# Kernel tuning notes

Hardware: AMD Instinct MI355X
Metric: run time of the kernel (lower is better)

## Reference

```python
import jax, jax.numpy as jnp
import numpy as np

SEQ_LEN = 131072
NUM_NODES = 256
NUM_CAUSES = 16
NUM_FEATURES = 100
NUM_OUTPUTS = 1
NOISE_STD = 0.01


def _build_dag_mask(N, C, p, rng):
    # upper-triangular random adjacency; roots (0..C-1) have no parents;
    # every non-root gets at least one parent (mirrors _build_random_dag)
    A = (rng.random((N, N)) < p) & np.triu(np.ones((N, N), bool), k=1)
    A[:, :C] = False
    for j in range(C, N):
        if not A[:j, j].any():
            A[rng.integers(0, j), j] = True
    return A.astype(np.int32)


def setup_inputs() -> dict:
    key = jax.random.key(0)
    k1, k2, k3 = jax.random.split(key, 3)
    rng = np.random.default_rng(0)
    S, N, C = SEQ_LEN, NUM_NODES, NUM_CAUSES
    causes = jax.random.normal(k1, (S, C), dtype=jnp.float32)
    W = jax.random.normal(k2, (N, N), dtype=jnp.float32)  # edge weights w_ij ~ N(0,1)
    eps = jax.random.normal(k3, (S, N - C), dtype=jnp.float32)  # unit noise, scaled by NOISE_STD
    mask = jnp.asarray(_build_dag_mask(N, C, 0.3, rng))
    act_id = jnp.asarray(rng.integers(0, 4, size=(N - C,)), dtype=jnp.int32)
    # y from a sink-like last node; X from sorted sample of remaining non-root nodes
    y_idx = jnp.asarray([N - 1], dtype=jnp.int64)
    X_idx = jnp.asarray(np.sort(rng.choice(np.arange(C, N - 1), size=NUM_FEATURES, replace=False)), dtype=jnp.int64)
    return {"causes": causes, "W": W, "eps": eps, "mask": mask, "act_id": act_id, "X_idx": X_idx, "y_idx": y_idx}


def reference(causes, W, eps, mask, act_id, X_idx, y_idx):
    S, C = causes.shape
    N = W.shape[0]
    Wm = W * mask.astype(W.dtype)                      # [N,N] masked edge weights (parent i -> node j)
    vals0 = jnp.zeros((S, N), W.dtype).at[:, :C].set(causes)
    Wcols = Wm.T[C:]                                   # [N-C, N] incoming-weight rows per non-root node
    eps_t = eps.T                                      # [N-C, S]
    branches = [lambda z: z, jnp.tanh, jax.nn.relu, jax.nn.sigmoid]

    def step(carry, xs):
        vals, idx = carry
        w_col, e, a = xs
        z = vals @ w_col + jnp.float32(NOISE_STD) * e  # weighted parent sum + noise, [S]
        v = jax.lax.switch(a, branches, z)
        vals = vals.at[:, idx].set(v)
        return (vals, idx + 1), None

    (vals, _), _ = jax.lax.scan(step, (vals0, jnp.int32(C)), (Wcols, eps_t, act_id))
    X = vals[:, X_idx]                                 # [S, num_features]
    y = vals[:, y_idx]                                 # [S, 1]
    bad = jnp.isnan(X).any() | jnp.isnan(y).any()
    X = jnp.where(bad, jnp.float32(0.0), X)
    y = jnp.where(bad, jnp.float32(-100.0), y)
    return X, y[:, 0]                                  # num_outputs == 1 -> squeeze
```

## Files before the change

kernel.cpp:

```cpp
#include <hip/hip_runtime.h>
#include <hip/hip_bf16.h>
#include <hip/hip_fp16.h>


typedef _Float16 half8 __attribute__((ext_vector_type(8)));
typedef float    f32x4 __attribute__((ext_vector_type(4)));

constexpr int S_LEN    = 131072;
constexpr int N_NODES  = 256;
constexpr int N_CAUSES = 16;
constexpr int N_COMP   = 240;
constexpr int N_FEAT   = 100;
constexpr float NOISE  = 0.01f;
constexpr float VSC    = 0.0625f;
constexpr float VSCI   = 16.0f;

constexpr int KE_tab[16]  = {0,32,64,64,96,96,128,128,160,160,192,192,224,224,256,256};
constexpr int OFF_tab[16] = {0,0,1024,3072,5120,8192,11264,15360,19456,24576,29696,
                             35840,41984,49152,56320,64512};

__constant__ int c_KE[16]  = {0,32,64,64,96,96,128,128,160,160,192,192,224,224,256,256};
__constant__ int c_OFF[16] = {0,0,1024,3072,5120,8192,11264,15360,19456,24576,29696,
                              35840,41984,49152,56320,64512};

__device__ _Float16 g_WT[72704];
__device__ float    g_Wtri[15 * 256];

__device__ __forceinline__ bool sniff_binary64(const void* p) {
    const unsigned* u = (const unsigned*)p;
    bool ok = true;
    for (int i = 0; i < 64; ++i) ok = ok && (u[i] <= 1u);
    return ok;
}
__device__ __forceinline__ bool sniff_is_bf16(const void* p) {
    const unsigned* u = (const unsigned*)p;
    bool ok = true;
    for (int i = 0; i < 16; ++i) {
        unsigned e = ((u[i] << 16) >> 23) & 0xffu;
        ok = ok && (e >= 100u) && (e <= 132u);
    }
    return ok;
}
__device__ __forceinline__ float bflo(unsigned u) { return __uint_as_float(u << 16); }
__device__ __forceinline__ float bfhi(unsigned u) { return __uint_as_float(u & 0xffff0000u); }

__device__ __forceinline__ void load16(const void* base, long long off, bool isbf, float* o) {
    if (isbf) {
        const uint4* p = (const uint4*)((const unsigned short*)base + off);
        uint4 a = p[0], b = p[1];
        o[0]=bflo(a.x); o[1]=bfhi(a.x); o[2]=bflo(a.y); o[3]=bfhi(a.y);
        o[4]=bflo(a.z); o[5]=bfhi(a.z); o[6]=bflo(a.w); o[7]=bfhi(a.w);
        o[8]=bflo(b.x); o[9]=bfhi(b.x); o[10]=bflo(b.y); o[11]=bfhi(b.y);
        o[12]=bflo(b.z); o[13]=bfhi(b.z); o[14]=bflo(b.w); o[15]=bfhi(b.w);
    } else {
        const float4* p = (const float4*)((const float*)base + off);
        float4 x0=p[0], x1=p[1], x2=p[2], x3=p[3];
        o[0]=x0.x; o[1]=x0.y; o[2]=x0.z; o[3]=x0.w;
        o[4]=x1.x; o[5]=x1.y; o[6]=x1.z; o[7]=x1.w;
        o[8]=x2.x; o[9]=x2.y; o[10]=x2.z; o[11]=x2.w;
        o[12]=x3.x; o[13]=x3.y; o[14]=x3.z; o[15]=x3.w;
    }
}

__device__ __forceinline__ float hw_exp2(float x) {
    float r; asm("v_exp_f32 %0, %1" : "=v"(r) : "v"(x)); return r;
}
__device__ __forceinline__ float hw_rcp(float x) {
    float r; asm("v_rcp_f32 %0, %1" : "=v"(r) : "v"(x)); return r;
}
__device__ __forceinline__ float fast_tanh(float x) {
    float t = hw_exp2(x * 2.88539008177792681f);
    return 1.0f - 2.0f * hw_rcp(t + 1.0f);
}
__device__ __forceinline__ float fast_sigmoid(float x) {
    return hw_rcp(1.0f + hw_exp2(x * -1.44269504088896341f));
}

__global__ void prep_kernel(const void* __restrict__ A, const void* __restrict__ B) {
    __shared__ int s_mA, s_wbf;
    if (threadIdx.x == 0) {
        s_mA  = sniff_binary64(A) ? 1 : 0;
        s_wbf = sniff_is_bf16(s_mA ? B : A) ? 1 : 0;
    }
    __syncthreads();
    const int*  maskp = (const int*)(s_mA ? A : B);
    const void* Wp    = s_mA ? B : A;
    const int k = blockIdx.x + 1, j0 = 16 * k, KE = c_KE[k], OFF = c_OFF[k];
    const int tid = threadIdx.x;

    for (int n = 0; n < 16; ++n) {
        const int j = j0 + n;
        for (int kk = tid; kk < KE; kk += 256) {
            const int gi = kk * N_NODES + j;
            float w = 0.0f;
            if (maskp[gi])
                w = s_wbf ? __bfloat162float(((const __hip_bfloat16*)Wp)[gi])
                          : ((const float*)Wp)[gi];
            const _Float16 hi = (_Float16)w;
            const _Float16 lo = (_Float16)(w - (float)hi);
            g_WT[OFF + n * KE + kk]           = hi;
            g_WT[OFF + 16 * KE + n * KE + kk] = lo;
        }
    }
    {
        const int l = tid >> 4, i = tid & 15;
        const int gi = (j0 + l) * N_NODES + (j0 + i);
        float w = 0.0f;
        if (l < i && maskp[gi])
            w = s_wbf ? __bfloat162float(((const __hip_bfloat16*)Wp)[gi])
                      : ((const float*)Wp)[gi];
        g_Wtri[(k - 1) * 256 + tid] = w;
    }
}

#define MFMA16(a, b, c) __builtin_amdgcn_mfma_f32_16x16x32_f16((a), (b), (c), 0, 0, 0)

template<int K>
__device__ __forceinline__ void do_chunk(
    const int lane, const long long sg,
    const void* __restrict__ eps, const bool ebf,
    half8 (&vf)[2][8],
    half8 (&bufA)[16], half8 (&bufB)[16],
    float* __restrict__ Zbuf, _Float16* __restrict__ stag,
    const short* __restrict__ xpos, const int* __restrict__ act_id,
    float* __restrict__ wsX,
    float* __restrict__ outX, float* __restrict__ outY, const int yi)
{
    constexpr int j0  = 16 * K;
    constexpr int KE  = KE_tab[K];
    constexpr int NST = KE / 32;

    const int mrow = lane & 15;
    const int quad = lane >> 4;

    half8 (&bc)[16] = *((K & 1) ? &bufA : &bufB);
    half8 (&bn)[16] = *((K & 1) ? &bufB : &bufA);

    float ev[16];
    if (lane < 32)
        load16(eps, sg * (long long)N_COMP + (j0 - N_CAUSES), ebf, ev);

    f32x4 acc0h = {0.f,0.f,0.f,0.f}, acc0l = {0.f,0.f,0.f,0.f};
    f32x4 acc1h = {0.f,0.f,0.f,0.f}, acc1l = {0.f,0.f,0.f,0.f};

    #pragma unroll
    for (int t = 0; t < NST; ++t) {
        acc0h = MFMA16(vf[0][t], bc[t],     acc0h);
        acc1h = MFMA16(vf[1][t], bc[t],     acc1h);
        acc0l = MFMA16(vf[0][t], bc[8 + t], acc0l);
        acc1l = MFMA16(vf[1][t], bc[8 + t], acc1l);
    }

    if constexpr (K < 15) {
        constexpr int KN  = K + 1;
        constexpr int KEn = KE_tab[KN];
        constexpr int NSTn = KEn / 32;
        constexpr int OFFn = OFF_tab[KN];
        const _Float16* __restrict__ bpn = g_WT + OFFn + mrow * KEn + (quad << 3);
        #pragma unroll
        for (int t = 0; t < NSTn; ++t) {
            bn[t]     = *(const half8*)(bpn + (t << 5));
            bn[8 + t] = *(const half8*)(bpn + 16 * KEn + (t << 5));
        }
    }

    {
        const int r0 = quad << 2;
        #pragma unroll
        for (int r = 0; r < 4; ++r) {
            Zbuf[(r0 + r)      * 21 + mrow] = (acc0h[r] + acc0l[r]) * VSCI;
            Zbuf[(16 + r0 + r) * 21 + mrow] = (acc1h[r] + acc1l[r]) * VSCI;
        }
    }
    __builtin_amdgcn_wave_barrier();

    if (lane < 32) {
        float zz[16];
        #pragma unroll
        for (int i = 0; i < 16; ++i)
            zz[i] = Zbuf[lane * 21 + i] + NOISE * ev[i];

        const float* __restrict__ tri = g_Wtri + (K - 1) * 256;
        half8 h0, h1;
        #pragma unroll
        for (int i = 0; i < 16; ++i) {
            float z = zz[i];
            const int a = act_id[j0 - N_CAUSES + i];
            if (a == 1)      z = fast_tanh(z);
            else if (a == 2) z = fmaxf(z, 0.0f);
            else if (a == 3) z = fast_sigmoid(z);
            if (i < 8) h0[i] = (_Float16)(z * VSC);
            else       h1[i - 8] = (_Float16)(z * VSC);
            const int xp = xpos[j0 - N_CAUSES + i];
            if (xp >= 0) {
                if (wsX) wsX[(long long)xp * S_LEN + sg] = z;
                else     outX[xp] = z;
            }
            if (j0 + i == yi) outY[sg] = z;
            #pragma unroll
            for (int j = i + 1; j < 16; ++j)
                zz[j] += tri[(i << 4) + j] * z;
        }
        *(half8*)(stag + lane * 24)     = h0;
        *(half8*)(stag + lane * 24 + 8) = h1;
    }
    __builtin_amdgcn_wave_barrier();

    constexpr int TT = K >> 1;
    constexpr int HB = (K & 1) << 1;
    if (quad == HB || quad == HB + 1) {
        const int boff = (quad - HB) << 3;
        #pragma unroll
        for (int q = 0; q < 2; ++q)
            vf[q][TT] = *(const half8*)(stag + (q * 16 + mrow) * 24 + boff);
    }
    __builtin_amdgcn_wave_barrier();
}

__global__ __launch_bounds__(64, 2)
void scm_kernel(const void* __restrict__ causes,
                const void* __restrict__ eps,
                const int* __restrict__ act_id,
                const void* __restrict__ xidx_raw,
                const int* __restrict__ yidx_raw,
                float* __restrict__ out,
                float* __restrict__ wsX,
                long long ybase) {
    __shared__ __align__(16) float    Zbuf[32 * 21];
    __shared__ __align__(16) _Float16 stag[32 * 24];
    __shared__ short xpos[N_COMP];

    const int lane = threadIdx.x;
    const long long sg = (long long)blockIdx.x * 32 + lane;

    for (int t = lane; t < N_COMP; t += 64) xpos[t] = -1;
    const unsigned long long* x64 = (const unsigned long long*)xidx_raw;
    const int*                x32 = (const int*)xidx_raw;
    const bool is64 = ((x64[0] >> 32) == 0ull);
    __builtin_amdgcn_wave_barrier();
    for (int f = lane; f < N_FEAT; f += 64) {
        const int ix = is64 ? (int)x64[f] : x32[f];
        xpos[ix - N_CAUSES] = (short)f;
    }
    __builtin_amdgcn_wave_barrier();
    const int yi  = yidx_raw[0];
    const bool cbf = sniff_is_bf16(causes);
    const bool ebf = sniff_is_bf16(eps);

    const int mrow = lane & 15;
    const int quad = lane >> 4;

    half8 vz;
    #pragma unroll
    for (int e = 0; e < 8; ++e) vz[e] = (_Float16)0.0f;
    half8 vf[2][8];
    #pragma unroll
    for (int q = 0; q < 2; ++q) {
        #pragma unroll
        for (int t = 0; t < 8; ++t) vf[q][t] = vz;
    }

    half8 bufA[16], bufB[16];
    #pragma unroll
    for (int t = 0; t < 16; ++t) { bufA[t] = vz; bufB[t] = vz; }

    {
        const _Float16* __restrict__ bp1 =
            g_WT + OFF_tab[1] + mrow * KE_tab[1] + (quad << 3);
        bufA[0] = *(const half8*)(bp1);
        bufA[8] = *(const half8*)(bp1 + 16 * KE_tab[1]);
    }

    if (lane < 32) {
        float cv[16];
        load16(causes, sg * (long long)N_CAUSES, cbf, cv);
        half8 c0, c1;
        #pragma unroll
        for (int i = 0; i < 8; ++i) {
            c0[i] = (_Float16)(cv[i] * VSC);
            c1[i] = (_Float16)(cv[8 + i] * VSC);
        }
        *(half8*)(stag + lane * 24)     = c0;
        *(half8*)(stag + lane * 24 + 8) = c1;
    }
    __builtin_amdgcn_wave_barrier();
    if (quad < 2) {
        #pragma unroll
        for (int q = 0; q < 2; ++q)
            vf[q][0] = *(const half8*)(stag + (q * 16 + mrow) * 24 + (quad << 3));
    }
    __builtin_amdgcn_wave_barrier();

    float* outX = out + sg * N_FEAT;
    float* outY = out + ybase;

    do_chunk< 1>(lane, sg, eps, ebf, vf, bufA, bufB, Zbuf, stag, xpos, act_id, wsX, outX, outY, yi);
    do_chunk< 2>(lane, sg, eps, ebf, vf, bufA, bufB, Zbuf, stag, xpos, act_id, wsX, outX, outY, yi);
    do_chunk< 3>(lane, sg, eps, ebf, vf, bufA, bufB, Zbuf, stag, xpos, act_id, wsX, outX, outY, yi);
    do_chunk< 4>(lane, sg, eps, ebf, vf, bufA, bufB, Zbuf, stag, xpos, act_id, wsX, outX, outY, yi);
    do_chunk< 5>(lane, sg, eps, ebf, vf, bufA, bufB, Zbuf, stag, xpos, act_id, wsX, outX, outY, yi);
    do_chunk< 6>(lane, sg, eps, ebf, vf, bufA, bufB, Zbuf, stag, xpos, act_id, wsX, outX, outY, yi);
    do_chunk< 7>(lane, sg, eps, ebf, vf, bufA, bufB, Zbuf, stag, xpos, act_id, wsX, outX, outY, yi);
    do_chunk< 8>(lane, sg, eps, ebf, vf, bufA, bufB, Zbuf, stag, xpos, act_id, wsX, outX, outY, yi);
    do_chunk< 9>(lane, sg, eps, ebf, vf, bufA, bufB, Zbuf, stag, xpos, act_id, wsX, outX, outY, yi);
    do_chunk<10>(lane, sg, eps, ebf, vf, bufA, bufB, Zbuf, stag, xpos, act_id, wsX, outX, outY, yi);
    do_chunk<11>(lane, sg, eps, ebf, vf, bufA, bufB, Zbuf, stag, xpos, act_id, wsX, outX, outY, yi);
    do_chunk<12>(lane, sg, eps, ebf, vf, bufA, bufB, Zbuf, stag, xpos, act_id, wsX, outX, outY, yi);
    do_chunk<13>(lane, sg, eps, ebf, vf, bufA, bufB, Zbuf, stag, xpos, act_id, wsX, outX, outY, yi);
    do_chunk<14>(lane, sg, eps, ebf, vf, bufA, bufB, Zbuf, stag, xpos, act_id, wsX, outX, outY, yi);
    do_chunk<15>(lane, sg, eps, ebf, vf, bufA, bufB, Zbuf, stag, xpos, act_id, wsX, outX, outY, yi);
}

__global__ __launch_bounds__(256)
void xpose_kernel(const float* __restrict__ ws, float* __restrict__ out) {
    __shared__ float tile[64 * 108];
    const int tid = threadIdx.x;
    const long long s0 = (long long)blockIdx.x * 64;
    #pragma unroll
    for (int g = 0; g < 7; ++g) {
        const int idx = g * 256 + tid;
        if (idx < 1600) {
            const int ff = idx >> 4;
            const int sl = idx & 15;
            const float4 v = *(const float4*)(ws + (long long)ff * S_LEN + s0 + sl * 4);
            tile[(sl * 4 + 0) * 108 + ff] = v.x;
            tile[(sl * 4 + 1) * 108 + ff] = v.y;
            tile[(sl * 4 + 2) * 108 + ff] = v.z;
            tile[(sl * 4 + 3) * 108 + ff] = v.w;
        }
    }
    __syncthreads();
    #pragma unroll
    for (int g = 0; g < 7; ++g) {
        const int idx = g * 256 + tid;
        if (idx < 1600) {
            const int s = idx / 25;
            const int j = idx % 25;
            const float4 v = *(const float4*)(tile + s * 108 + j * 4);
            *(float4*)(out + (s0 + s) * N_FEAT + j * 4) = v;
        }
    }
}

extern "C" void kernel_launch(void* const* d_in, const int* in_sizes, int n_in,
                              void* d_out, int out_size, void* d_ws, size_t ws_size,
                              hipStream_t stream) {
    int ic = 0, iw = 1, ie = 2, im = 3, ia = 4, ix = 5, iy = 6;
    int c = -1, e = -1, a = -1, x = -1, y = -1, m1 = -1, m2 = -1;
    for (int i = 0; i < n_in; ++i) {
        switch (in_sizes[i]) {
            case S_LEN * N_CAUSES:   c = i; break;
            case S_LEN * N_COMP:     e = i; break;
            case N_COMP:             a = i; break;
            case N_FEAT:             x = i; break;
            case 1:                  y = i; break;
            case N_NODES * N_NODES:  (m1 < 0 ? m1 : m2) = i; break;
        }
    }
    if (c >= 0 && e >= 0 && a >= 0 && x >= 0 && y >= 0 && m1 >= 0 && m2 >= 0) {
        ic = c; ie = e; ia = a; ix = x; iy = y; iw = m1; im = m2;
    }

    const void* causes = d_in[ic];
    const void* TA     = d_in[iw];
    const void* TB     = d_in[im];
    const void* eps    = d_in[ie];
    const int*  act_id = (const int*)d_in[ia];
    const void* xidx   = d_in[ix];
    const int*  yidx   = (const int*)d_in[iy];
    float*      out    = (float*)d_out;
    const long long ybase = (long long)out_size - S_LEN;

    const bool usews = ws_size >= (size_t)N_FEAT * S_LEN * sizeof(float);
    float* wsX = usews ? (float*)d_ws : nullptr;

    prep_kernel<<<15, 256, 0, stream>>>(TA, TB);
    scm_kernel<<<S_LEN / 32, 64, 0, stream>>>(causes, eps, act_id, xidx, yidx,
                                              out, wsX, ybase);
    if (usews)
        xpose_kernel<<<S_LEN / 64, 256, 0, stream>>>(wsX, out);
}
```

Measured before the change: 371.2 us.

## Drop register double-buffered weights, stage triangular weights and activation ids in LDS

Removes the two 16-entry half8 register buffers that prefetched the next chunk's MFMA B operands. Weights are now loaded directly inside the MFMA loop, and the launch bound is raised to request four waves per SIMD instead of two. The per-chunk 16x16 triangular weights are prefetched one chunk ahead into a double-buffered LDS array, and activation ids are cached in LDS as shorts, so the sequential intra-chunk solve reads LDS instead of global memory. This trades the explicit prefetch, and the load latency it hid, for higher occupancy and lower register pressure.

```diff
diff --git a/kernel.cpp b/kernel.cpp
--- a/kernel.cpp
+++ b/kernel.cpp
@@ -120,48 +120,41 @@
     const int lane, const long long sg,
     const void* __restrict__ eps, const bool ebf,
     half8 (&vf)[2][8],
-    half8 (&bufA)[16], half8 (&bufB)[16],
     float* __restrict__ Zbuf, _Float16* __restrict__ stag,
-    const short* __restrict__ xpos, const int* __restrict__ act_id,
+    float (&trib)[2][256],
+    const short* __restrict__ xpos, const short* __restrict__ acts,
     float* __restrict__ wsX,
     float* __restrict__ outX, float* __restrict__ outY, const int yi)
 {
     constexpr int j0  = 16 * K;
     constexpr int KE  = KE_tab[K];
     constexpr int NST = KE / 32;
+    constexpr int OFF = OFF_tab[K];
 
     const int mrow = lane & 15;
     const int quad = lane >> 4;
 
-    half8 (&bc)[16] = *((K & 1) ? &bufA : &bufB);
-    half8 (&bn)[16] = *((K & 1) ? &bufB : &bufA);
+    float4 trv;
+    if constexpr (K < 15)
+        trv = *(const float4*)(g_Wtri + K * 256 + lane * 4);
 
     float ev[16];
     if (lane < 32)
         load16(eps, sg * (long long)N_COMP + (j0 - N_CAUSES), ebf, ev);
 
+    const _Float16* __restrict__ bp = g_WT + OFF + mrow * KE + (quad << 3);
+
     f32x4 acc0h = {0.f,0.f,0.f,0.f}, acc0l = {0.f,0.f,0.f,0.f};
     f32x4 acc1h = {0.f,0.f,0.f,0.f}, acc1l = {0.f,0.f,0.f,0.f};
 
     #pragma unroll
     for (int t = 0; t < NST; ++t) {
-        acc0h = MFMA16(vf[0][t], bc[t],     acc0h);
-        acc1h = MFMA16(vf[1][t], bc[t],     acc1h);
-        acc0l = MFMA16(vf[0][t], bc[8 + t], acc0l);
-        acc1l = MFMA16(vf[1][t], bc[8 + t], acc1l);
-    }
-
-    if constexpr (K < 15) {
-        constexpr int KN  = K + 1;
-        constexpr int KEn = KE_tab[KN];
-        constexpr int NSTn = KEn / 32;
-        constexpr int OFFn = OFF_tab[KN];
-        const _Float16* __restrict__ bpn = g_WT + OFFn + mrow * KEn + (quad << 3);
-        #pragma unroll
-        for (int t = 0; t < NSTn; ++t) {
-            bn[t]     = *(const half8*)(bpn + (t << 5));
-            bn[8 + t] = *(const half8*)(bpn + 16 * KEn + (t << 5));
-        }
+        const half8 bh = *(const half8*)(bp + (t << 5));
+        const half8 bl = *(const half8*)(bp + 16 * KE + (t << 5));
+        acc0h = MFMA16(vf[0][t], bh, acc0h);
+        acc1h = MFMA16(vf[1][t], bh, acc1h);
+        acc0l = MFMA16(vf[0][t], bl, acc0l);
+        acc1l = MFMA16(vf[1][t], bl, acc1l);
     }
 
     {
@@ -172,6 +165,8 @@
             Zbuf[(16 + r0 + r) * 21 + mrow] = (acc1h[r] + acc1l[r]) * VSCI;
         }
     }
+    if constexpr (K < 15)
+        *(float4*)(&trib[(K + 1) & 1][lane * 4]) = trv;
     __builtin_amdgcn_wave_barrier();
 
     if (lane < 32) {
@@ -180,12 +175,12 @@
         for (int i = 0; i < 16; ++i)
             zz[i] = Zbuf[lane * 21 + i] + NOISE * ev[i];
 
-        const float* __restrict__ tri = g_Wtri + (K - 1) * 256;
+        const float* __restrict__ tri = &trib[K & 1][0];
         half8 h0, h1;
         #pragma unroll
         for (int i = 0; i < 16; ++i) {
             float z = zz[i];
-            const int a = act_id[j0 - N_CAUSES + i];
+            const int a = acts[j0 - N_CAUSES + i];
             if (a == 1)      z = fast_tanh(z);
             else if (a == 2) z = fmaxf(z, 0.0f);
             else if (a == 3) z = fast_sigmoid(z);
@@ -217,7 +212,7 @@
     __builtin_amdgcn_wave_barrier();
 }
 
-__global__ __launch_bounds__(64, 2)
+__global__ __launch_bounds__(64, 4)
 void scm_kernel(const void* __restrict__ causes,
                 const void* __restrict__ eps,
                 const int* __restrict__ act_id,
@@ -228,12 +223,17 @@
                 long long ybase) {
     __shared__ __align__(16) float    Zbuf[32 * 21];
     __shared__ __align__(16) _Float16 stag[32 * 24];
+    __shared__ __align__(16) float    trib[2][256];
     __shared__ short xpos[N_COMP];
+    __shared__ short acts[N_COMP];
 
     const int lane = threadIdx.x;
     const long long sg = (long long)blockIdx.x * 32 + lane;
 
-    for (int t = lane; t < N_COMP; t += 64) xpos[t] = -1;
+    for (int t = lane; t < N_COMP; t += 64) {
+        xpos[t] = -1;
+        acts[t] = (short)act_id[t];
+    }
     const unsigned long long* x64 = (const unsigned long long*)xidx_raw;
     const int*                x32 = (const int*)xidx_raw;
     const bool is64 = ((x64[0] >> 32) == 0ull);
@@ -250,6 +250,11 @@
     const int mrow = lane & 15;
     const int quad = lane >> 4;
 
+    {
+        const float4 tv = *(const float4*)(g_Wtri + lane * 4);
+        *(float4*)(&trib[1][lane * 4]) = tv;
+    }
+
     half8 vz;
     #pragma unroll
     for (int e = 0; e < 8; ++e) vz[e] = (_Float16)0.0f;
@@ -258,17 +263,6 @@
     for (int q = 0; q < 2; ++q) {
         #pragma unroll
         for (int t = 0; t < 8; ++t) vf[q][t] = vz;
-    }
-
-    half8 bufA[16], bufB[16];
-    #pragma unroll
-    for (int t = 0; t < 16; ++t) { bufA[t] = vz; bufB[t] = vz; }
-
-    {
-        const _Float16* __restrict__ bp1 =
-            g_WT + OFF_tab[1] + mrow * KE_tab[1] + (quad << 3);
-        bufA[0] = *(const half8*)(bp1);
-        bufA[8] = *(const half8*)(bp1 + 16 * KE_tab[1]);
     }
 
     if (lane < 32) {
@@ -294,21 +288,21 @@
     float* outX = out + sg * N_FEAT;
     float* outY = out + ybase;
 
-    do_chunk< 1>(lane, sg, eps, ebf, vf, bufA, bufB, Zbuf, stag, xpos, act_id, wsX, outX, outY, yi);
-    do_chunk< 2>(lane, sg, eps, ebf, vf, bufA, bufB, Zbuf, stag, xpos, act_id, wsX, outX, outY, yi);
-    do_chunk< 3>(lane, sg, eps, ebf, vf, bufA, bufB, Zbuf, stag, xpos, act_id, wsX, outX, outY, yi);
-    do_chunk< 4>(lane, sg, eps, ebf, vf, bufA, bufB, Zbuf, stag, xpos, act_id, wsX, outX, outY, yi);
-    do_chunk< 5>(lane, sg, eps, ebf, vf, bufA, bufB, Zbuf, stag, xpos, act_id, wsX, outX, outY, yi);
-    do_chunk< 6>(lane, sg, eps, ebf, vf, bufA, bufB, Zbuf, stag, xpos, act_id, wsX, outX, outY, yi);
-    do_chunk< 7>(lane, sg, eps, ebf, vf, bufA, bufB, Zbuf, stag, xpos, act_id, wsX, outX, outY, yi);
-    do_chunk< 8>(lane, sg, eps, ebf, vf, bufA, bufB, Zbuf, stag, xpos, act_id, wsX, outX, outY, yi);
-    do_chunk< 9>(lane, sg, eps, ebf, vf, bufA, bufB, Zbuf, stag, xpos, act_id, wsX, outX, outY, yi);
-    do_chunk<10>(lane, sg, eps, ebf, vf, bufA, bufB, Zbuf, stag, xpos, act_id, wsX, outX, outY, yi);
-    do_chunk<11>(lane, sg, eps, ebf, vf, bufA, bufB, Zbuf, stag, xpos, act_id, wsX, outX, outY, yi);
-    do_chunk<12>(lane, sg, eps, ebf, vf, bufA, bufB, Zbuf, stag, xpos, act_id, wsX, outX, outY, yi);
-    do_chunk<13>(lane, sg, eps, ebf, vf, bufA, bufB, Zbuf, stag, xpos, act_id, wsX, outX, outY, yi);
-    do_chunk<14>(lane, sg, eps, ebf, vf, bufA, bufB, Zbuf, stag, xpos, act_id, wsX, outX, outY, yi);
-    do_chunk<15>(lane, sg, eps, ebf, vf, bufA, bufB, Zbuf, stag, xpos, act_id, wsX, outX, outY, yi);
+    do_chunk< 1>(lane, sg, eps, ebf, vf, Zbuf, stag, trib, xpos, acts, wsX, outX, outY, yi);
+    do_chunk< 2>(lane, sg, eps, ebf, vf, Zbuf, stag, trib, xpos, acts, wsX, outX, outY, yi);
+    do_chunk< 3>(lane, sg, eps, ebf, vf, Zbuf, stag, trib, xpos, acts, wsX, outX, outY, yi);
+    do_chunk< 4>(lane, sg, eps, ebf, vf, Zbuf, stag, trib, xpos, acts, wsX, outX, outY, yi);
+    do_chunk< 5>(lane, sg, eps, ebf, vf, Zbuf, stag, trib, xpos, acts, wsX, outX, outY, yi);
+    do_chunk< 6>(lane, sg, eps, ebf, vf, Zbuf, stag, trib, xpos, acts, wsX, outX, outY, yi);
+    do_chunk< 7>(lane, sg, eps, ebf, vf, Zbuf, stag, trib, xpos, acts, wsX, outX, outY, yi);
+    do_chunk< 8>(lane, sg, eps, ebf, vf, Zbuf, stag, trib, xpos, acts, wsX, outX, outY, yi);
+    do_chunk< 9>(lane, sg, eps, ebf, vf, Zbuf, stag, trib, xpos, acts, wsX, outX, outY, yi);
+    do_chunk<10>(lane, sg, eps, ebf, vf, Zbuf, stag, trib, xpos, acts, wsX, outX, outY, yi);
+    do_chunk<11>(lane, sg, eps, ebf, vf, Zbuf, stag, trib, xpos, acts, wsX, outX, outY, yi);
+    do_chunk<12>(lane, sg, eps, ebf, vf, Zbuf, stag, trib, xpos, acts, wsX, outX, outY, yi);
+    do_chunk<13>(lane, sg, eps, ebf, vf, Zbuf, stag, trib, xpos, acts, wsX, outX, outY, yi);
+    do_chunk<14>(lane, sg, eps, ebf, vf, Zbuf, stag, trib, xpos, acts, wsX, outX, outY, yi);
+    do_chunk<15>(lane, sg, eps, ebf, vf, Zbuf, stag, trib, xpos, acts, wsX, outX, outY, yi);
 }
 
 __global__ __launch_bounds__(256)
```

Result: faster. 343.7 us (-7.4%).
